# Performance work log

Hardware: AMD Instinct MI355X
Metric: run time of the kernel (lower is better)

Reference implementation:

```python
import jax, jax.numpy as jnp
import numpy as np

B, T, D, H = 8, 256, 12, 4
NQ = 12                      # n_qubits_ffn == ffn_dim
NL_ATTN, NL_FFN = 2, 2
EPS = 1e-5
C64 = jnp.complex64


def _z_signs(n):
    # [n, 2**n] sign table: wire 0 is the most-significant bit of the flat index
    idx = np.arange(2 ** n)
    bits = (idx[None, :] >> (n - 1 - np.arange(n)[:, None])) & 1
    return jnp.asarray(1 - 2 * bits, dtype=jnp.float32)


def _apply_1q(state, gate, n, w):
    # state [N, 2**n]; gate [2,2] (shared) or [N,2,2] (per-token)
    a, b = 2 ** w, 2 ** (n - w - 1)
    s = state.reshape(-1, a, 2, b)
    if gate.ndim == 2:
        s = jnp.einsum('ij,najb->naib', gate, s)
    else:
        s = jnp.einsum('nij,najb->naib', gate, s)
    return s.reshape(-1, 2 ** n)


def _apply_cnot(state, n, c, t):
    s = state.reshape((-1,) + (2,) * n)
    ac, at = 1 + c, 1 + t
    s0 = jnp.take(s, 0, axis=ac)
    s1 = jnp.take(s, 1, axis=ac)
    s1 = jnp.flip(s1, axis=at - 1 if at > ac else at)  # flip target where control==1
    s = jnp.stack([s0, s1], axis=ac)
    return s.reshape(-1, 2 ** n)


def _rx_batched(theta):  # theta [N] -> [N,2,2]
    c = jnp.cos(theta / 2).astype(C64)
    s = jnp.sin(theta / 2).astype(C64)
    return jnp.stack([c, -1j * s, -1j * s, c], axis=-1).reshape(-1, 2, 2)


def _rx_scalar(theta):
    c = jnp.cos(theta / 2).astype(C64)
    s = jnp.sin(theta / 2).astype(C64)
    return jnp.stack([c, -1j * s, -1j * s, c]).reshape(2, 2)


def _ry_scalar(theta):
    c = jnp.cos(theta / 2)
    s = jnp.sin(theta / 2)
    return jnp.stack([c, -s, s, c]).reshape(2, 2).astype(C64)


def _qcircuit(angles, thetas, n, n_layers, param_gate):
    # angles [N, n] encoder RX rotations; thetas [n] trainable gate params
    N = angles.shape[0]
    state = jnp.zeros((N, 2 ** n), C64).at[:, 0].set(1.0)
    for w in range(n):                       # GeneralEncoder: RX(x_w) on wire w
        state = _apply_1q(state, _rx_batched(angles[:, w]), n, w)
    for w in range(n):                       # trainable RX/RY per wire
        state = _apply_1q(state, param_gate(thetas[w]), n, w)
    for _ in range(n_layers - 1):            # CNOT entangling ring
        for w in range(n - 1):
            state = _apply_cnot(state, n, w, w + 1)
        state = _apply_cnot(state, n, n - 1, 0)
    probs = jnp.abs(state) ** 2
    return probs @ _z_signs(n).T             # MeasureAll(PauliZ) -> [N, n]


def _layer_norm(x, g, b):
    m = x.mean(-1, keepdims=True)
    v = ((x - m) ** 2).mean(-1, keepdims=True)
    return (x - m) * jax.lax.rsqrt(v + EPS) * g + b


def _mha(x, mask, Wi, bi, Wo, bo):
    qkv = x @ Wi.T + bi
    q, k, v = jnp.split(qkv, 3, axis=-1)
    hd = D // H
    sh = lambda t: t.reshape(B, T, H, hd).transpose(0, 2, 1, 3)
    q, k, v = sh(q), sh(k), sh(v)
    scores = jnp.einsum('bhqd,bhkd->bhqk', q, k) / float(np.sqrt(hd))
    scores = jnp.where(mask[:, None, None, :] != 0, -jnp.inf, scores)
    attn = jax.nn.softmax(scores, axis=-1)
    out = jnp.einsum('bhqk,bhkd->bhqd', attn, v).transpose(0, 2, 1, 3).reshape(B, T, D)
    return out @ Wo.T + bo


def setup_inputs() -> dict:
    key = jax.random.key(0)
    ks = jax.random.split(key, 12)
    g = lambda i, shape, sc: (jax.random.normal(ks[i], shape, jnp.float32) * sc)
    return {
        'x': jax.random.normal(ks[0], (B, T, D), jnp.float32),
        'in_proj_w': g(1, (3 * D, D), 0.3),
        'in_proj_b': g(2, (3 * D,), 0.02),
        'out_proj_w': g(3, (D, D), 0.3),
        'out_proj_b': g(4, (D,), 0.02),
        'attn_theta': jax.random.uniform(ks[5], (D,), jnp.float32, -np.pi, np.pi),
        'lin1_w': g(6, (NQ, D), 0.3),
        'lin1_b': g(7, (NQ,), 0.02),
        'ffn_theta': jax.random.uniform(ks[8], (NQ,), jnp.float32, -np.pi, np.pi),
        'lin2_w': g(9, (D, NQ), 0.3),
        'lin2_b': g(10, (D,), 0.02),
        'ln1_g': jnp.ones((D,), jnp.float32),
        'ln1_b': jnp.zeros((D,), jnp.float32),
        'ln2_g': jnp.ones((D,), jnp.float32),
        'ln2_b': jnp.zeros((D,), jnp.float32),
        'mask': jnp.zeros((B, T), jnp.int32),
    }


def reference(x, in_proj_w, in_proj_b, out_proj_w, out_proj_b, attn_theta,
              lin1_w, lin1_b, ffn_theta, lin2_w, lin2_b,
              ln1_g, ln1_b, ln2_g, ln2_b, mask):
    # quantum multi-head attention (dropout/noise are identity in eval)
    attn_cls = _mha(x, mask, in_proj_w, in_proj_b, out_proj_w, out_proj_b)
    attn_q = _qcircuit(attn_cls.reshape(B * T, D), attn_theta, D, NL_ATTN,
                       _rx_scalar).reshape(B, T, D)
    x1 = _layer_norm(x + attn_q, ln1_g, ln1_b)
    # quantum feed-forward
    q_in = x1 @ lin1_w.T + lin1_b                       # [B,T,NQ]
    ffn_q = _qcircuit(q_in.reshape(B * T, NQ), ffn_theta, NQ, NL_FFN,
                      _ry_scalar).reshape(B, T, NQ)
    ffn_out = jax.nn.relu(ffn_q @ lin2_w.T + lin2_b)    # [B,T,D]
    return _layer_norm(x1 + ffn_out, ln2_g, ln2_b)
```

## Files before the change

kernel.cpp:

```cpp
#include <hip/hip_runtime.h>
#include <math.h>

#define BB 8
#define TT 256
#define DD 12
#define HH 4
#define HDIM 3
#define MASK_NEG -3.0e38f

__global__ __launch_bounds__(TT) void attn_kernel(
    const float* __restrict__ x,
    const float* __restrict__ wi,
    const float* __restrict__ bi,
    const int*   __restrict__ mask,
    float* __restrict__ headout)
{
    const int b = blockIdx.x / HH;
    const int h = blockIdx.x % HH;
    const int t = threadIdx.x;

    __shared__ float4 kk4[TT];
    __shared__ float4 vv4[TT];

    const float4* xr4 = (const float4*)(x + (b * TT + t) * DD);
    const float4 p0 = xr4[0], p1 = xr4[1], p2 = xr4[2];
    const float xv[DD] = {p0.x, p0.y, p0.z, p0.w, p1.x, p1.y, p1.z, p1.w,
                          p2.x, p2.y, p2.z, p2.w};

    float q[HDIM], kx[HDIM], vx[HDIM];
#pragma unroll
    for (int d = 0; d < HDIM; ++d) {
        const int rq = h * HDIM + d;
        const int rk = DD + h * HDIM + d;
        const int rv = 2 * DD + h * HDIM + d;
        float aq = bi[rq], ak = bi[rk], av = bi[rv];
#pragma unroll
        for (int j = 0; j < DD; ++j) {
            aq = fmaf(wi[rq * DD + j], xv[j], aq);
            ak = fmaf(wi[rk * DD + j], xv[j], ak);
            av = fmaf(wi[rv * DD + j], xv[j], av);
        }
        q[d] = aq; kx[d] = ak; vx[d] = av;
    }
    const float mb = (mask[b * TT + t] != 0) ? MASK_NEG : 0.0f;
    kk4[t] = make_float4(kx[0], kx[1], kx[2], mb);
    vv4[t] = make_float4(vx[0], vx[1], vx[2], 0.0f);
    __syncthreads();

    const float scale = 0.57735026918962576f;
    const float qs0 = q[0] * scale, qs1 = q[1] * scale, qs2 = q[2] * scale;

    float mA = MASK_NEG, sumA = 0.f, aA0 = 0.f, aA1 = 0.f, aA2 = 0.f;
    float mB = MASK_NEG, sumB = 0.f, aB0 = 0.f, aB1 = 0.f, aB2 = 0.f;
#pragma unroll 4
    for (int k = 0; k < TT / 2; ++k) {
        const float4 kA = kk4[k];
        const float4 kB = kk4[k + TT / 2];
        const float sA = fmaf(qs0, kA.x, fmaf(qs1, kA.y, qs2 * kA.z)) + kA.w;
        const float sB = fmaf(qs0, kB.x, fmaf(qs1, kB.y, qs2 * kB.z)) + kB.w;
        const float4 vA = vv4[k];
        const float4 vB = vv4[k + TT / 2];

        const float mAn = fmaxf(mA, sA);
        const float cA  = __expf(mA - mAn);
        const float eA  = __expf(sA - mAn);
        sumA = fmaf(sumA, cA, eA);
        aA0 = fmaf(aA0, cA, eA * vA.x);
        aA1 = fmaf(aA1, cA, eA * vA.y);
        aA2 = fmaf(aA2, cA, eA * vA.z);
        mA = mAn;

        const float mBn = fmaxf(mB, sB);
        const float cB  = __expf(mB - mBn);
        const float eB  = __expf(sB - mBn);
        sumB = fmaf(sumB, cB, eB);
        aB0 = fmaf(aB0, cB, eB * vB.x);
        aB1 = fmaf(aB1, cB, eB * vB.y);
        aB2 = fmaf(aB2, cB, eB * vB.z);
        mB = mBn;
    }
    const float m  = fmaxf(mA, mB);
    const float cA = __expf(mA - m), cB = __expf(mB - m);
    const float sum = sumA * cA + sumB * cB;
    const float inv = 1.0f / sum;
    float* orow = headout + (b * TT + t) * DD + h * HDIM;
    orow[0] = (aA0 * cA + aB0 * cB) * inv;
    orow[1] = (aA1 * cA + aB1 * cB) * inv;
    orow[2] = (aA2 * cA + aB2 * cB) * inv;
}

__device__ __forceinline__ void ring_measure(const float* z, float* outp)
{
    float pref = 1.0f;
#pragma unroll
    for (int j = 0; j < DD; ++j) { pref *= z[j]; outp[j] = pref; }
    float suf = 1.0f;
#pragma unroll
    for (int j = 1; j < DD; ++j) suf *= z[j];
    outp[0] = suf;
}

__device__ __forceinline__ void layer_norm(float* v, const float* __restrict__ g,
                                           const float* __restrict__ b)
{
    float mean = 0.f;
#pragma unroll
    for (int j = 0; j < DD; ++j) mean += v[j];
    mean *= (1.0f / DD);
    float var = 0.f;
#pragma unroll
    for (int j = 0; j < DD; ++j) { float d = v[j] - mean; var = fmaf(d, d, var); }
    var *= (1.0f / DD);
    const float r = rsqrtf(var + 1e-5f);
#pragma unroll
    for (int j = 0; j < DD; ++j) v[j] = (v[j] - mean) * r * g[j] + b[j];
}

__global__ __launch_bounds__(64) void fused_tail_kernel(
    const float* __restrict__ x,
    const float* __restrict__ headout,
    const float* __restrict__ wo, const float* __restrict__ bo,
    const float* __restrict__ th_a,
    const float* __restrict__ w1, const float* __restrict__ b1,
    const float* __restrict__ th_f,
    const float* __restrict__ w2, const float* __restrict__ b2,
    const float* __restrict__ g1, const float* __restrict__ be1,
    const float* __restrict__ g2, const float* __restrict__ be2,
    float* __restrict__ out)
{
    const int n = blockIdx.x * blockDim.x + threadIdx.x;
    if (n >= BB * TT) return;

    const float4* hr4 = (const float4*)(headout + n * DD);
    const float4 h0 = hr4[0], h1 = hr4[1], h2 = hr4[2];
    const float hv[DD] = {h0.x, h0.y, h0.z, h0.w, h1.x, h1.y, h1.z, h1.w,
                          h2.x, h2.y, h2.z, h2.w};

    float ac[DD];
#pragma unroll
    for (int d = 0; d < DD; ++d) {
        float a = bo[d];
#pragma unroll
        for (int j = 0; j < DD; ++j) a = fmaf(wo[d * DD + j], hv[j], a);
        ac[d] = a;
    }

    float z[DD], aq[DD];
#pragma unroll
    for (int j = 0; j < DD; ++j) z[j] = __cosf(ac[j] + th_a[j]);
    ring_measure(z, aq);

    const float4* xr4 = (const float4*)(x + n * DD);
    const float4 x0 = xr4[0], x1q = xr4[1], x2q = xr4[2];
    float x1[DD] = {x0.x, x0.y, x0.z, x0.w, x1q.x, x1q.y, x1q.z, x1q.w,
                    x2q.x, x2q.y, x2q.z, x2q.w};
#pragma unroll
    for (int j = 0; j < DD; ++j) x1[j] += aq[j];
    layer_norm(x1, g1, be1);

    float qi[DD];
#pragma unroll
    for (int d = 0; d < DD; ++d) {
        float a = b1[d];
#pragma unroll
        for (int j = 0; j < DD; ++j) a = fmaf(w1[d * DD + j], x1[j], a);
        qi[d] = a;
    }

    float fq[DD];
#pragma unroll
    for (int j = 0; j < DD; ++j) z[j] = __cosf(th_f[j]) * __cosf(qi[j]);
    ring_measure(z, fq);

    float y[DD];
#pragma unroll
    for (int d = 0; d < DD; ++d) {
        float a = b2[d];
#pragma unroll
        for (int j = 0; j < DD; ++j) a = fmaf(w2[d * DD + j], fq[j], a);
        y[d] = fmaxf(a, 0.0f) + x1[d];
    }
    layer_norm(y, g2, be2);

    float4* or4 = (float4*)(out + n * DD);
    or4[0] = make_float4(y[0], y[1], y[2],  y[3]);
    or4[1] = make_float4(y[4], y[5], y[6],  y[7]);
    or4[2] = make_float4(y[8], y[9], y[10], y[11]);
}

extern "C" void kernel_launch(void* const* d_in, const int* in_sizes, int n_in,
                              void* d_out, int out_size, void* d_ws, size_t ws_size,
                              hipStream_t stream)
{
    const float* x    = (const float*)d_in[0];
    const float* wi   = (const float*)d_in[1];
    const float* bi   = (const float*)d_in[2];
    const float* wo   = (const float*)d_in[3];
    const float* bo   = (const float*)d_in[4];
    const float* tha  = (const float*)d_in[5];
    const float* w1   = (const float*)d_in[6];
    const float* b1   = (const float*)d_in[7];
    const float* thf  = (const float*)d_in[8];
    const float* w2   = (const float*)d_in[9];
    const float* b2   = (const float*)d_in[10];
    const float* g1   = (const float*)d_in[11];
    const float* be1  = (const float*)d_in[12];
    const float* g2   = (const float*)d_in[13];
    const float* be2  = (const float*)d_in[14];
    const int*   mask = (const int*)d_in[15];
    float* out = (float*)d_out;
    float* headout = (float*)d_ws;

    attn_kernel<<<BB * HH, TT, 0, stream>>>(x, wi, bi, mask, headout);
    fused_tail_kernel<<<(BB * TT + 63) / 64, 64, 0, stream>>>(
        x, headout, wo, bo, tha, w1, b1, thf, w2, b2, g1, be1, g2, be2, out);
}
```

Baseline: 103.5 us.

## Split attention keys across blocks and merge partial softmax sums in tail kernel

The attention kernel now splits the 256 keys into 4 chunks, so it launches four times as many blocks. Each block projects only its own chunk of K/V and writes an unnormalized partial (sum, weighted V) per query and head. The tail kernel adds the four partials and normalizes them before the output projection. The running-max online softmax is dropped and exp is applied to raw scores. This shortens the serial loop and removes its extra exps, but it can overflow if scores grow large, and it needs a larger workspace.

New measurement: 94.64 us, median of 2. -8.5%, faster.

```diff
diff --git a/kernel.cpp b/kernel.cpp
--- a/kernel.cpp
+++ b/kernel.cpp
@@ -6,87 +6,79 @@
 #define DD 12
 #define HH 4
 #define HDIM 3
+#define KSPLIT 4
+#define KCHUNK (TT / KSPLIT)
 #define MASK_NEG -3.0e38f
 
-__global__ __launch_bounds__(TT) void attn_kernel(
+__global__ __launch_bounds__(TT) void attn_partial_kernel(
     const float* __restrict__ x,
     const float* __restrict__ wi,
     const float* __restrict__ bi,
     const int*   __restrict__ mask,
-    float* __restrict__ headout)
-{
-    const int b = blockIdx.x / HH;
-    const int h = blockIdx.x % HH;
+    float4* __restrict__ part)
+{
+    const int bh = blockIdx.x >> 2;
+    const int kq = blockIdx.x & 3;
+    const int b = bh / HH;
+    const int h = bh % HH;
     const int t = threadIdx.x;
 
-    __shared__ float4 kk4[TT];
-    __shared__ float4 vv4[TT];
+    __shared__ float4 kk4[KCHUNK];
+    __shared__ float4 vv4[KCHUNK];
+
+    if (t < KCHUNK) {
+        const int key = kq * KCHUNK + t;
+        const float4* kr4 = (const float4*)(x + (b * TT + key) * DD);
+        const float4 c0 = kr4[0], c1 = kr4[1], c2 = kr4[2];
+        const float kvv[DD] = {c0.x, c0.y, c0.z, c0.w, c1.x, c1.y, c1.z, c1.w,
+                               c2.x, c2.y, c2.z, c2.w};
+        float kx[HDIM], vx[HDIM];
+#pragma unroll
+        for (int d = 0; d < HDIM; ++d) {
+            const int rk = DD + h * HDIM + d;
+            const int rv = 2 * DD + h * HDIM + d;
+            float ak = bi[rk], av = bi[rv];
+#pragma unroll
+            for (int j = 0; j < DD; ++j) {
+                ak = fmaf(wi[rk * DD + j], kvv[j], ak);
+                av = fmaf(wi[rv * DD + j], kvv[j], av);
+            }
+            kx[d] = ak; vx[d] = av;
+        }
+        const float mb = (mask[b * TT + key] != 0) ? MASK_NEG : 0.0f;
+        kk4[t] = make_float4(kx[0], kx[1], kx[2], mb);
+        vv4[t] = make_float4(vx[0], vx[1], vx[2], 0.0f);
+    }
 
     const float4* xr4 = (const float4*)(x + (b * TT + t) * DD);
     const float4 p0 = xr4[0], p1 = xr4[1], p2 = xr4[2];
     const float xv[DD] = {p0.x, p0.y, p0.z, p0.w, p1.x, p1.y, p1.z, p1.w,
                           p2.x, p2.y, p2.z, p2.w};
-
-    float q[HDIM], kx[HDIM], vx[HDIM];
+    const float scale = 0.57735026918962576f;
+    float qs[HDIM];
 #pragma unroll
     for (int d = 0; d < HDIM; ++d) {
         const int rq = h * HDIM + d;
-        const int rk = DD + h * HDIM + d;
-        const int rv = 2 * DD + h * HDIM + d;
-        float aq = bi[rq], ak = bi[rk], av = bi[rv];
-#pragma unroll
-        for (int j = 0; j < DD; ++j) {
-            aq = fmaf(wi[rq * DD + j], xv[j], aq);
-            ak = fmaf(wi[rk * DD + j], xv[j], ak);
-            av = fmaf(wi[rv * DD + j], xv[j], av);
-        }
-        q[d] = aq; kx[d] = ak; vx[d] = av;
-    }
-    const float mb = (mask[b * TT + t] != 0) ? MASK_NEG : 0.0f;
-    kk4[t] = make_float4(kx[0], kx[1], kx[2], mb);
-    vv4[t] = make_float4(vx[0], vx[1], vx[2], 0.0f);
+        float a = bi[rq];
+#pragma unroll
+        for (int j = 0; j < DD; ++j) a = fmaf(wi[rq * DD + j], xv[j], a);
+        qs[d] = a * scale;
+    }
     __syncthreads();
 
-    const float scale = 0.57735026918962576f;
-    const float qs0 = q[0] * scale, qs1 = q[1] * scale, qs2 = q[2] * scale;
-
-    float mA = MASK_NEG, sumA = 0.f, aA0 = 0.f, aA1 = 0.f, aA2 = 0.f;
-    float mB = MASK_NEG, sumB = 0.f, aB0 = 0.f, aB1 = 0.f, aB2 = 0.f;
-#pragma unroll 4
-    for (int k = 0; k < TT / 2; ++k) {
-        const float4 kA = kk4[k];
-        const float4 kB = kk4[k + TT / 2];
-        const float sA = fmaf(qs0, kA.x, fmaf(qs1, kA.y, qs2 * kA.z)) + kA.w;
-        const float sB = fmaf(qs0, kB.x, fmaf(qs1, kB.y, qs2 * kB.z)) + kB.w;
-        const float4 vA = vv4[k];
-        const float4 vB = vv4[k + TT / 2];
-
-        const float mAn = fmaxf(mA, sA);
-        const float cA  = __expf(mA - mAn);
-        const float eA  = __expf(sA - mAn);
-        sumA = fmaf(sumA, cA, eA);
-        aA0 = fmaf(aA0, cA, eA * vA.x);
-        aA1 = fmaf(aA1, cA, eA * vA.y);
-        aA2 = fmaf(aA2, cA, eA * vA.z);
-        mA = mAn;
-
-        const float mBn = fmaxf(mB, sB);
-        const float cB  = __expf(mB - mBn);
-        const float eB  = __expf(sB - mBn);
-        sumB = fmaf(sumB, cB, eB);
-        aB0 = fmaf(aB0, cB, eB * vB.x);
-        aB1 = fmaf(aB1, cB, eB * vB.y);
-        aB2 = fmaf(aB2, cB, eB * vB.z);
-        mB = mBn;
-    }
-    const float m  = fmaxf(mA, mB);
-    const float cA = __expf(mA - m), cB = __expf(mB - m);
-    const float sum = sumA * cA + sumB * cB;
-    const float inv = 1.0f / sum;
-    float* orow = headout + (b * TT + t) * DD + h * HDIM;
-    orow[0] = (aA0 * cA + aB0 * cB) * inv;
-    orow[1] = (aA1 * cA + aB1 * cB) * inv;
-    orow[2] = (aA2 * cA + aB2 * cB) * inv;
+    float sum = 0.f, a0 = 0.f, a1 = 0.f, a2 = 0.f;
+#pragma unroll
+    for (int k = 0; k < KCHUNK; ++k) {
+        const float4 kk = kk4[k];
+        const float4 vv = vv4[k];
+        const float s = fmaf(qs[0], kk.x, fmaf(qs[1], kk.y, fmaf(qs[2], kk.z, kk.w)));
+        const float e = __expf(s);
+        sum += e;
+        a0 = fmaf(e, vv.x, a0);
+        a1 = fmaf(e, vv.y, a1);
+        a2 = fmaf(e, vv.z, a2);
+    }
+    part[((b * TT + t) * HH + h) * KSPLIT + kq] = make_float4(sum, a0, a1, a2);
 }
 
 __device__ __forceinline__ void ring_measure(const float* z, float* outp)
@@ -118,7 +110,7 @@
 
 __global__ __launch_bounds__(64) void fused_tail_kernel(
     const float* __restrict__ x,
-    const float* __restrict__ headout,
+    const float4* __restrict__ part,
     const float* __restrict__ wo, const float* __restrict__ bo,
     const float* __restrict__ th_a,
     const float* __restrict__ w1, const float* __restrict__ b1,
@@ -131,10 +123,20 @@
     const int n = blockIdx.x * blockDim.x + threadIdx.x;
     if (n >= BB * TT) return;
 
-    const float4* hr4 = (const float4*)(headout + n * DD);
-    const float4 h0 = hr4[0], h1 = hr4[1], h2 = hr4[2];
-    const float hv[DD] = {h0.x, h0.y, h0.z, h0.w, h1.x, h1.y, h1.z, h1.w,
-                          h2.x, h2.y, h2.z, h2.w};
+    float hv[DD];
+    const float4* pp = part + n * HH * KSPLIT;
+#pragma unroll
+    for (int h = 0; h < HH; ++h) {
+        const float4 q0 = pp[h * KSPLIT + 0];
+        const float4 q1 = pp[h * KSPLIT + 1];
+        const float4 q2 = pp[h * KSPLIT + 2];
+        const float4 q3 = pp[h * KSPLIT + 3];
+        const float s  = (q0.x + q1.x) + (q2.x + q3.x);
+        const float inv = __builtin_amdgcn_rcpf(s);
+        hv[h * HDIM + 0] = ((q0.y + q1.y) + (q2.y + q3.y)) * inv;
+        hv[h * HDIM + 1] = ((q0.z + q1.z) + (q2.z + q3.z)) * inv;
+        hv[h * HDIM + 2] = ((q0.w + q1.w) + (q2.w + q3.w)) * inv;
+    }
 
     float ac[DD];
 #pragma unroll
@@ -209,9 +211,9 @@
     const float* be2  = (const float*)d_in[14];
     const int*   mask = (const int*)d_in[15];
     float* out = (float*)d_out;
-    float* headout = (float*)d_ws;
-
-    attn_kernel<<<BB * HH, TT, 0, stream>>>(x, wi, bi, mask, headout);
+    float4* part = (float4*)d_ws;
+
+    attn_partial_kernel<<<BB * HH * KSPLIT, TT, 0, stream>>>(x, wi, bi, mask, part);
     fused_tail_kernel<<<(BB * TT + 63) / 64, 64, 0, stream>>>(
-        x, headout, wo, bo, tha, w1, b1, thf, w2, b2, g1, be1, g2, be2, out);
-}
+        x, part, wo, bo, tha, w1, b1, thf, w2, b2, g1, be1, g2, be2, out);
+}
```
